# Kernel tuning notes

Hardware: AMD Instinct MI355X
Metric: run time of the kernel (lower is better)

## Reference

```python
import jax, jax.numpy as jnp
import numpy as np

N_NODES = 100000
N_EDGES = 1600000
Z_DIM = 64
EDGE_FEAT_DIM = 16
HIDDEN = 128


def setup_inputs() -> dict:
    key = jax.random.key(0)
    k_z, k_ei, k_ea, k_w1, k_b1, k_w2, k_b2 = jax.random.split(key, 7)
    in_dim = 2 * Z_DIM + EDGE_FEAT_DIM
    return {
        "z": jax.random.normal(k_z, (N_NODES, Z_DIM), dtype=jnp.float32),
        "edge_index": jax.random.randint(k_ei, (2, N_EDGES), 0, N_NODES, dtype=jnp.int64),
        "edge_attr": jax.random.normal(k_ea, (N_EDGES, EDGE_FEAT_DIM), dtype=jnp.float32),
        # decoder_mlp params: Linear(2*z_dim+edge_feat_dim, 128) -> ReLU -> Linear(128, 1)
        "W1": jax.random.normal(k_w1, (in_dim, HIDDEN), dtype=jnp.float32) / np.float32(np.sqrt(in_dim)),
        "b1": jax.random.normal(k_b1, (HIDDEN,), dtype=jnp.float32) * 0.01,
        "W2": jax.random.normal(k_w2, (HIDDEN, 1), dtype=jnp.float32) / np.float32(np.sqrt(HIDDEN)),
        "b2": jax.random.normal(k_b2, (1,), dtype=jnp.float32) * 0.01,
    }


def reference(z, edge_index, edge_attr, W1, b1, W2, b2):
    # decode(): gather endpoint embeddings, concat edge features, 2-layer MLP, sigmoid
    src = edge_index[0]
    dst = edge_index[1]
    edge_input = jnp.concatenate([z[src], z[dst], edge_attr], axis=1)  # [E, 2Z+F]
    h = jax.nn.relu(edge_input @ W1 + b1)  # [E, 128]
    logits = h @ W2 + b2                   # [E, 1]
    return jax.nn.sigmoid(logits).squeeze(-1)  # [E]
```

## Files before the change

kernel.cpp:

```cpp
#include <hip/hip_runtime.h>

#define EDGES 1600000
#define NN    100000
#define ZD    64
#define FD    16
#define HID   128
#define BM    64
#define THREADS 256
#define NBLK  1250
#define TPW   5
#define KSTEPS 10
#define NFRAG 2560
#define WT_SHORTS (NFRAG * 8)

typedef __attribute__((ext_vector_type(8)))  short bfrag;
typedef __attribute__((ext_vector_type(16))) float f16v;

__device__ __forceinline__ unsigned short f2bf(float f) {
  unsigned u = __builtin_bit_cast(unsigned, f);
  u += 0x7fffu + ((u >> 16) & 1u);
  return (unsigned short)(u >> 16);
}
__device__ __forceinline__ unsigned cvtpk(float lo, float hi) {
  unsigned r;
  asm("v_cvt_pk_bf16_f32 %0, %1, %2" : "=v"(r) : "v"(lo), "v"(hi));
  return r;
}
__device__ __forceinline__ void gload16(const void* g, void* l) {
  __builtin_amdgcn_global_load_lds(
      (const __attribute__((address_space(1))) unsigned int*)g,
      (__attribute__((address_space(3))) unsigned int*)l, 16, 0, 0);
}

__global__ void zconv_kernel(const float* __restrict__ z,
                             unsigned short* __restrict__ z16, int n4) {
  int i = blockIdx.x * blockDim.x + threadIdx.x;
  if (i >= n4) return;
  float4 f = reinterpret_cast<const float4*>(z)[i];
  ushort4 p;
  p.x = f2bf(f.x); p.y = f2bf(f.y); p.z = f2bf(f.z); p.w = f2bf(f.w);
  reinterpret_cast<ushort4*>(z16)[i] = p;
}

__global__ void wtab_kernel(const float* __restrict__ W1,
                            const float* __restrict__ b1,
                            unsigned short* __restrict__ WT) {
  int i = blockIdx.x * blockDim.x + threadIdx.x;
  if (i >= WT_SHORTS) return;
  int j    = i & 7;
  int frag = i >> 3;
  int lane = frag & 63;
  int s    = (frag >> 6) % KSTEPS;
  int blk  = frag / (KSTEPS * 64);
  int hid  = blk * 32 + (lane & 31);
  int k    = s * 16 + (lane >> 5) * 8 + j;
  float v = (k < 144) ? W1[k * HID + hid] : (k == 144 ? b1[hid] : 0.f);
  WT[i] = f2bf(v);
}

template<bool ZB>
__global__ __launch_bounds__(THREADS, 2) void fused_kernel(
    const float* __restrict__ zf, const unsigned short* __restrict__ z16,
    const unsigned short* __restrict__ WT,
    const int* __restrict__ ei, const float* __restrict__ ea,
    const float* __restrict__ W2, const float* __restrict__ b2,
    float* __restrict__ out)
{
  __shared__ __align__(16) int4 sW[NFRAG];
  __shared__ __align__(16) float sW2[HID];

  const int tid  = threadIdx.x;
  const int lane = tid & 63;
  const int wid  = tid >> 6;
  const int e    = lane & 31;
  const int hi   = lane >> 5;

  #pragma unroll
  for (int c = 0; c < 10; ++c)
    gload16(WT + (size_t)(c * 256 + tid) * 8, &sW[c * 256 + tid]);
  if (tid < HID) sW2[tid] = W2[tid];
  asm volatile("s_waitcnt vmcnt(0)" ::: "memory");
  __syncthreads();

  const float bias2 = b2[0];

  int4 oq = {0, 0, 0, 0};
  if (hi == 0) oq.x = 0x3F80;
  const bfrag cone = __builtin_bit_cast(bfrag, oq);

  f16v zerov;
  #pragma unroll
  for (int rg = 0; rg < 16; ++rg) zerov[rg] = 0.f;

#define GZ(x0, x1, x2, x3, x4, x5, x6, x7, xa, xb, si, di, ebase) do {         \
    if constexpr (ZB) {                                                        \
      const unsigned short* ps_ = z16 + (size_t)(si) * ZD + hi * 8;            \
      const unsigned short* pd_ = z16 + (size_t)(di) * ZD + hi * 8;            \
      x0 = *reinterpret_cast<const bfrag*>(ps_);                               \
      x1 = *reinterpret_cast<const bfrag*>(ps_ + 16);                          \
      x2 = *reinterpret_cast<const bfrag*>(ps_ + 32);                          \
      x3 = *reinterpret_cast<const bfrag*>(ps_ + 48);                          \
      x4 = *reinterpret_cast<const bfrag*>(pd_);                               \
      x5 = *reinterpret_cast<const bfrag*>(pd_ + 16);                          \
      x6 = *reinterpret_cast<const bfrag*>(pd_ + 32);                          \
      x7 = *reinterpret_cast<const bfrag*>(pd_ + 48);                          \
    } else {                                                                   \
      const float* ps_ = zf + (size_t)(si) * ZD + hi * 8;                      \
      const float* pd_ = zf + (size_t)(di) * ZD + hi * 8;                      \
      float4 a_, b_;                                                           \
      a_ = ((const float4*)ps_)[0]; b_ = ((const float4*)ps_)[1];              \
      { int4 q_ = {(int)cvtpk(a_.x,a_.y),(int)cvtpk(a_.z,a_.w),                \
                   (int)cvtpk(b_.x,b_.y),(int)cvtpk(b_.z,b_.w)};               \
        x0 = __builtin_bit_cast(bfrag, q_); }                                  \
      a_ = ((const float4*)(ps_+16))[0]; b_ = ((const float4*)(ps_+16))[1];    \
      { int4 q_ = {(int)cvtpk(a_.x,a_.y),(int)cvtpk(a_.z,a_.w),                \
                   (int)cvtpk(b_.x,b_.y),(int)cvtpk(b_.z,b_.w)};               \
        x1 = __builtin_bit_cast(bfrag, q_); }                                  \
      a_ = ((const float4*)(ps_+32))[0]; b_ = ((const float4*)(ps_+32))[1];    \
      { int4 q_ = {(int)cvtpk(a_.x,a_.y),(int)cvtpk(a_.z,a_.w),                \
                   (int)cvtpk(b_.x,b_.y),(int)cvtpk(b_.z,b_.w)};               \
        x2 = __builtin_bit_cast(bfrag, q_); }                                  \
      a_ = ((const float4*)(ps_+48))[0]; b_ = ((const float4*)(ps_+48))[1];    \
      { int4 q_ = {(int)cvtpk(a_.x,a_.y),(int)cvtpk(a_.z,a_.w),                \
                   (int)cvtpk(b_.x,b_.y),(int)cvtpk(b_.z,b_.w)};               \
        x3 = __builtin_bit_cast(bfrag, q_); }                                  \
      a_ = ((const float4*)pd_)[0]; b_ = ((const float4*)pd_)[1];              \
      { int4 q_ = {(int)cvtpk(a_.x,a_.y),(int)cvtpk(a_.z,a_.w),                \
                   (int)cvtpk(b_.x,b_.y),(int)cvtpk(b_.z,b_.w)};               \
        x4 = __builtin_bit_cast(bfrag, q_); }                                  \
      a_ = ((const float4*)(pd_+16))[0]; b_ = ((const float4*)(pd_+16))[1];    \
      { int4 q_ = {(int)cvtpk(a_.x,a_.y),(int)cvtpk(a_.z,a_.w),                \
                   (int)cvtpk(b_.x,b_.y),(int)cvtpk(b_.z,b_.w)};               \
        x5 = __builtin_bit_cast(bfrag, q_); }                                  \
      a_ = ((const float4*)(pd_+32))[0]; b_ = ((const float4*)(pd_+32))[1];    \
      { int4 q_ = {(int)cvtpk(a_.x,a_.y),(int)cvtpk(a_.z,a_.w),                \
                   (int)cvtpk(b_.x,b_.y),(int)cvtpk(b_.z,b_.w)};               \
        x6 = __builtin_bit_cast(bfrag, q_); }                                  \
      a_ = ((const float4*)(pd_+48))[0]; b_ = ((const float4*)(pd_+48))[1];    \
      { int4 q_ = {(int)cvtpk(a_.x,a_.y),(int)cvtpk(a_.z,a_.w),                \
                   (int)cvtpk(b_.x,b_.y),(int)cvtpk(b_.z,b_.w)};               \
        x7 = __builtin_bit_cast(bfrag, q_); }                                  \
    }                                                                          \
    const float* pe_ = ea + (size_t)(ebase) * FD + hi * 8;                     \
    xa = ((const float4*)pe_)[0];                                              \
    xb = ((const float4*)pe_)[1];                                              \
  } while (0)

  const int gw = blockIdx.x * 4 + wid;
  const int T0 = gw * TPW;

  int sA = ei[(size_t)T0 * BM + e];
  int dA = ei[(size_t)EDGES + (size_t)T0 * BM + e];
  int sB = ei[(size_t)T0 * BM + 32 + e];
  int dB = ei[(size_t)EDGES + (size_t)T0 * BM + 32 + e];

  for (int t = 0; t < TPW; ++t) {
    const int tt = T0 + t;

    bfrag a0, a1, a2, a3, a4, a5, a6, a7; float4 aa, ab;
    GZ(a0, a1, a2, a3, a4, a5, a6, a7, aa, ab, sA, dA, (size_t)tt * BM + e);
    bfrag g0, g1, g2, g3, g4, g5, g6, g7; float4 ga, gb;
    GZ(g0, g1, g2, g3, g4, g5, g6, g7, ga, gb, sB, dB, (size_t)tt * BM + 32 + e);

    {
      const int tn = (t + 1 < TPW) ? tt + 1 : tt;
      sA = ei[(size_t)tn * BM + e];
      dA = ei[(size_t)EDGES + (size_t)tn * BM + e];
      sB = ei[(size_t)tn * BM + 32 + e];
      dB = ei[(size_t)EDGES + (size_t)tn * BM + 32 + e];
    }

    int4 eqa = {(int)cvtpk(aa.x, aa.y), (int)cvtpk(aa.z, aa.w),
                (int)cvtpk(ab.x, ab.y), (int)cvtpk(ab.z, ab.w)};
    bfrag a8 = __builtin_bit_cast(bfrag, eqa);
    int4 eqb = {(int)cvtpk(ga.x, ga.y), (int)cvtpk(ga.z, ga.w),
                (int)cvtpk(gb.x, gb.y), (int)cvtpk(gb.z, gb.w)};
    bfrag g8 = __builtin_bit_cast(bfrag, eqb);

    __builtin_amdgcn_s_setprio(1);
    float p0 = 0.f, p1 = 0.f, p2 = 0.f, p3 = 0.f;
    float q0 = 0.f, q1 = 0.f, q2 = 0.f, q3 = 0.f;
    #pragma unroll
    for (int blk = 0; blk < 4; ++blk) {
      const int4* wp = &sW[blk * (KSTEPS * 64) + lane];
      bfrag w0 = *reinterpret_cast<const bfrag*>(wp + 0 * 64);
      bfrag w1 = *reinterpret_cast<const bfrag*>(wp + 1 * 64);
      bfrag w2 = *reinterpret_cast<const bfrag*>(wp + 2 * 64);
      bfrag w3 = *reinterpret_cast<const bfrag*>(wp + 3 * 64);
      bfrag w4 = *reinterpret_cast<const bfrag*>(wp + 4 * 64);
      bfrag w5 = *reinterpret_cast<const bfrag*>(wp + 5 * 64);
      bfrag w6 = *reinterpret_cast<const bfrag*>(wp + 6 * 64);
      bfrag w7 = *reinterpret_cast<const bfrag*>(wp + 7 * 64);
      bfrag w8 = *reinterpret_cast<const bfrag*>(wp + 8 * 64);
      bfrag w9 = *reinterpret_cast<const bfrag*>(wp + 9 * 64);

      f16v accA;
      accA = __builtin_amdgcn_mfma_f32_32x32x16_bf16(w9, cone, zerov, 0, 0, 0);
      accA = __builtin_amdgcn_mfma_f32_32x32x16_bf16(w0, a0, accA, 0, 0, 0);
      accA = __builtin_amdgcn_mfma_f32_32x32x16_bf16(w1, a1, accA, 0, 0, 0);
      accA = __builtin_amdgcn_mfma_f32_32x32x16_bf16(w2, a2, accA, 0, 0, 0);
      accA = __builtin_amdgcn_mfma_f32_32x32x16_bf16(w3, a3, accA, 0, 0, 0);
      accA = __builtin_amdgcn_mfma_f32_32x32x16_bf16(w4, a4, accA, 0, 0, 0);
      accA = __builtin_amdgcn_mfma_f32_32x32x16_bf16(w5, a5, accA, 0, 0, 0);
      accA = __builtin_amdgcn_mfma_f32_32x32x16_bf16(w6, a6, accA, 0, 0, 0);
      accA = __builtin_amdgcn_mfma_f32_32x32x16_bf16(w7, a7, accA, 0, 0, 0);
      accA = __builtin_amdgcn_mfma_f32_32x32x16_bf16(w8, a8, accA, 0, 0, 0);

      f16v accB;
      accB = __builtin_amdgcn_mfma_f32_32x32x16_bf16(w9, cone, zerov, 0, 0, 0);
      accB = __builtin_amdgcn_mfma_f32_32x32x16_bf16(w0, g0, accB, 0, 0, 0);
      accB = __builtin_amdgcn_mfma_f32_32x32x16_bf16(w1, g1, accB, 0, 0, 0);
      accB = __builtin_amdgcn_mfma_f32_32x32x16_bf16(w2, g2, accB, 0, 0, 0);
      accB = __builtin_amdgcn_mfma_f32_32x32x16_bf16(w3, g3, accB, 0, 0, 0);
      accB = __builtin_amdgcn_mfma_f32_32x32x16_bf16(w4, g4, accB, 0, 0, 0);
      accB = __builtin_amdgcn_mfma_f32_32x32x16_bf16(w5, g5, accB, 0, 0, 0);
      accB = __builtin_amdgcn_mfma_f32_32x32x16_bf16(w6, g6, accB, 0, 0, 0);
      accB = __builtin_amdgcn_mfma_f32_32x32x16_bf16(w7, g7, accB, 0, 0, 0);
      accB = __builtin_amdgcn_mfma_f32_32x32x16_bf16(w8, g8, accB, 0, 0, 0);

      const float* wq = &sW2[blk * 32 + 4 * hi];
      float4 c0_ = *reinterpret_cast<const float4*>(wq);
      float4 c1_ = *reinterpret_cast<const float4*>(wq + 8);
      float4 c2_ = *reinterpret_cast<const float4*>(wq + 16);
      float4 c3_ = *reinterpret_cast<const float4*>(wq + 24);

      p0 = fmaf(fmaxf(accA[0],  0.f), c0_.x, p0);
      p1 = fmaf(fmaxf(accA[1],  0.f), c0_.y, p1);
      p2 = fmaf(fmaxf(accA[2],  0.f), c0_.z, p2);
      p3 = fmaf(fmaxf(accA[3],  0.f), c0_.w, p3);
      p0 = fmaf(fmaxf(accA[4],  0.f), c1_.x, p0);
      p1 = fmaf(fmaxf(accA[5],  0.f), c1_.y, p1);
      p2 = fmaf(fmaxf(accA[6],  0.f), c1_.z, p2);
      p3 = fmaf(fmaxf(accA[7],  0.f), c1_.w, p3);
      p0 = fmaf(fmaxf(accA[8],  0.f), c2_.x, p0);
      p1 = fmaf(fmaxf(accA[9],  0.f), c2_.y, p1);
      p2 = fmaf(fmaxf(accA[10], 0.f), c2_.z, p2);
      p3 = fmaf(fmaxf(accA[11], 0.f), c2_.w, p3);
      p0 = fmaf(fmaxf(accA[12], 0.f), c3_.x, p0);
      p1 = fmaf(fmaxf(accA[13], 0.f), c3_.y, p1);
      p2 = fmaf(fmaxf(accA[14], 0.f), c3_.z, p2);
      p3 = fmaf(fmaxf(accA[15], 0.f), c3_.w, p3);

      q0 = fmaf(fmaxf(accB[0],  0.f), c0_.x, q0);
      q1 = fmaf(fmaxf(accB[1],  0.f), c0_.y, q1);
      q2 = fmaf(fmaxf(accB[2],  0.f), c0_.z, q2);
      q3 = fmaf(fmaxf(accB[3],  0.f), c0_.w, q3);
      q0 = fmaf(fmaxf(accB[4],  0.f), c1_.x, q0);
      q1 = fmaf(fmaxf(accB[5],  0.f), c1_.y, q1);
      q2 = fmaf(fmaxf(accB[6],  0.f), c1_.z, q2);
      q3 = fmaf(fmaxf(accB[7],  0.f), c1_.w, q3);
      q0 = fmaf(fmaxf(accB[8],  0.f), c2_.x, q0);
      q1 = fmaf(fmaxf(accB[9],  0.f), c2_.y, q1);
      q2 = fmaf(fmaxf(accB[10], 0.f), c2_.z, q2);
      q3 = fmaf(fmaxf(accB[11], 0.f), c2_.w, q3);
      q0 = fmaf(fmaxf(accB[12], 0.f), c3_.x, q0);
      q1 = fmaf(fmaxf(accB[13], 0.f), c3_.y, q1);
      q2 = fmaf(fmaxf(accB[14], 0.f), c3_.z, q2);
      q3 = fmaf(fmaxf(accB[15], 0.f), c3_.w, q3);
    }
    __builtin_amdgcn_s_setprio(0);

    float p = (p0 + p1) + (p2 + p3);
    p += __shfl_xor(p, 32);
    float q = (q0 + q1) + (q2 + q3);
    q += __shfl_xor(q, 32);
    if (lane < 32) {
      out[(size_t)tt * BM + lane]      = 1.f / (1.f + __expf(-(p + bias2)));
      out[(size_t)tt * BM + 32 + lane] = 1.f / (1.f + __expf(-(q + bias2)));
    }
  }
#undef GZ
}

extern "C" void kernel_launch(void* const* d_in, const int* in_sizes, int n_in,
                              void* d_out, int out_size, void* d_ws, size_t ws_size,
                              hipStream_t stream) {
  const float* z  = (const float*)d_in[0];
  const int*   ei = (const int*)d_in[1];
  const float* ea = (const float*)d_in[2];
  const float* W1 = (const float*)d_in[3];
  const float* b1 = (const float*)d_in[4];
  const float* W2 = (const float*)d_in[5];
  const float* b2 = (const float*)d_in[6];
  float* out = (float*)d_out;

  const size_t z16_bytes = (size_t)NN * ZD * sizeof(unsigned short);
  const size_t wt_bytes  = (size_t)WT_SHORTS * sizeof(unsigned short);

  if (ws_size >= z16_bytes + wt_bytes) {
    unsigned short* z16 = (unsigned short*)d_ws;
    unsigned short* WT  = z16 + (size_t)NN * ZD;
    const int n4 = NN * ZD / 4;
    zconv_kernel<<<(n4 + 255) / 256, 256, 0, stream>>>(z, z16, n4);
    wtab_kernel<<<(WT_SHORTS + 255) / 256, 256, 0, stream>>>(W1, b1, WT);
    fused_kernel<true><<<NBLK, THREADS, 0, stream>>>(
        z, z16, WT, ei, ea, W2, b2, out);
  } else {
    unsigned short* WT = (unsigned short*)d_ws;
    wtab_kernel<<<(WT_SHORTS + 255) / 256, 256, 0, stream>>>(W1, b1, WT);
    fused_kernel<false><<<NBLK, THREADS, 0, stream>>>(
        z, nullptr, WT, ei, ea, W2, b2, out);
  }
}
```

Measured before the change: 98.36 us.

## Switch to persistent grid-stride tile loop with nontemporal streaming loads/stores

Replaces the fixed 1250-block grid with 5 contiguous tiles per wave by a 768-block persistent grid where each wave strides across all 25000 tiles. The aim is to cut block launch/tail overhead and amortize per-block setup such as loading weights into LDS. It also marks the streaming edge_index, edge_attr loads and output stores as nontemporal so they do not pollute the cache that serves the random z gathers. Waves now get uneven tile counts, which may cause tail imbalance, and the strided tile access loses some locality.

New measurement: 111.0 us. 12.8% more time.

```diff
diff --git a/kernel.cpp b/kernel.cpp
--- a/kernel.cpp
+++ b/kernel.cpp
@@ -7,14 +7,16 @@
 #define HID   128
 #define BM    64
 #define THREADS 256
-#define NBLK  1250
-#define TPW   5
+#define NBLK  768
+#define NT    25000
+#define WSTRIDE (NBLK * 4)
 #define KSTEPS 10
 #define NFRAG 2560
 #define WT_SHORTS (NFRAG * 8)
 
 typedef __attribute__((ext_vector_type(8)))  short bfrag;
 typedef __attribute__((ext_vector_type(16))) float f16v;
+typedef __attribute__((ext_vector_type(4)))  float f4v;
 
 __device__ __forceinline__ unsigned short f2bf(float f) {
   unsigned u = __builtin_bit_cast(unsigned, f);
@@ -141,33 +143,34 @@
                    (int)cvtpk(b_.x,b_.y),(int)cvtpk(b_.z,b_.w)};               \
         x7 = __builtin_bit_cast(bfrag, q_); }                                  \
     }                                                                          \
-    const float* pe_ = ea + (size_t)(ebase) * FD + hi * 8;                     \
-    xa = ((const float4*)pe_)[0];                                              \
-    xb = ((const float4*)pe_)[1];                                              \
+    const f4v* pe_ = (const f4v*)(ea + (size_t)(ebase) * FD + hi * 8);         \
+    xa = __builtin_nontemporal_load(pe_);                                      \
+    xb = __builtin_nontemporal_load(pe_ + 1);                                  \
   } while (0)
 
-  const int gw = blockIdx.x * 4 + wid;
-  const int T0 = gw * TPW;
-
-  int sA = ei[(size_t)T0 * BM + e];
-  int dA = ei[(size_t)EDGES + (size_t)T0 * BM + e];
-  int sB = ei[(size_t)T0 * BM + 32 + e];
-  int dB = ei[(size_t)EDGES + (size_t)T0 * BM + 32 + e];
-
-  for (int t = 0; t < TPW; ++t) {
-    const int tt = T0 + t;
-
-    bfrag a0, a1, a2, a3, a4, a5, a6, a7; float4 aa, ab;
+  const int gw  = blockIdx.x * 4 + wid;
+  const int nit = (NT - 1 - gw) / WSTRIDE + 1;
+
+  int tt0 = gw;
+  int sA = __builtin_nontemporal_load(ei + (size_t)tt0 * BM + e);
+  int dA = __builtin_nontemporal_load(ei + EDGES + (size_t)tt0 * BM + e);
+  int sB = __builtin_nontemporal_load(ei + (size_t)tt0 * BM + 32 + e);
+  int dB = __builtin_nontemporal_load(ei + EDGES + (size_t)tt0 * BM + 32 + e);
+
+  for (int t = 0; t < nit; ++t) {
+    const int tt = gw + t * WSTRIDE;
+
+    bfrag a0, a1, a2, a3, a4, a5, a6, a7; f4v aa, ab;
     GZ(a0, a1, a2, a3, a4, a5, a6, a7, aa, ab, sA, dA, (size_t)tt * BM + e);
-    bfrag g0, g1, g2, g3, g4, g5, g6, g7; float4 ga, gb;
+    bfrag g0, g1, g2, g3, g4, g5, g6, g7; f4v ga, gb;
     GZ(g0, g1, g2, g3, g4, g5, g6, g7, ga, gb, sB, dB, (size_t)tt * BM + 32 + e);
 
     {
-      const int tn = (t + 1 < TPW) ? tt + 1 : tt;
-      sA = ei[(size_t)tn * BM + e];
-      dA = ei[(size_t)EDGES + (size_t)tn * BM + e];
-      sB = ei[(size_t)tn * BM + 32 + e];
-      dB = ei[(size_t)EDGES + (size_t)tn * BM + 32 + e];
+      const int tn = (t + 1 < nit) ? tt + WSTRIDE : tt;
+      sA = __builtin_nontemporal_load(ei + (size_t)tn * BM + e);
+      dA = __builtin_nontemporal_load(ei + EDGES + (size_t)tn * BM + e);
+      sB = __builtin_nontemporal_load(ei + (size_t)tn * BM + 32 + e);
+      dB = __builtin_nontemporal_load(ei + EDGES + (size_t)tn * BM + 32 + e);
     }
 
     int4 eqa = {(int)cvtpk(aa.x, aa.y), (int)cvtpk(aa.z, aa.w),
@@ -265,8 +268,10 @@
     float q = (q0 + q1) + (q2 + q3);
     q += __shfl_xor(q, 32);
     if (lane < 32) {
-      out[(size_t)tt * BM + lane]      = 1.f / (1.f + __expf(-(p + bias2)));
-      out[(size_t)tt * BM + 32 + lane] = 1.f / (1.f + __expf(-(q + bias2)));
+      float vp = 1.f / (1.f + __expf(-(p + bias2)));
+      float vq = 1.f / (1.f + __expf(-(q + bias2)));
+      __builtin_nontemporal_store(vp, out + (size_t)tt * BM + lane);
+      __builtin_nontemporal_store(vq, out + (size_t)tt * BM + 32 + lane);
     }
   }
 #undef GZ
```
